# Kernel tuning notes

Hardware: AMD Instinct MI355X
Metric: run time of the kernel (lower is better)

## Reference

```python
import jax, jax.numpy as jnp
import numpy as np

N_META, M_SUB = 64, 1024          # n meta-nodes, m nodes per sub-graph
D_IN, D_HID, D_OUT = 128, 128, 64
NUM_LAYERS_EXTRA, K = 2, 3        # total DSGraphGLayers = NUM_LAYERS_EXTRA + 1
N_EDGES = 1048576                 # ~avg degree 16 over 65536 nodes


def setup_inputs() -> dict:
    key = jax.random.key(0)
    ks = jax.random.split(key, 8)
    N = N_META * M_SUB
    x = jax.random.normal(ks[0], (N_META, M_SUB, D_IN), jnp.float32)
    sub_adj = jax.random.randint(ks[1], (2, N_EDGES), 0, N, dtype=jnp.int32)
    # dense binary meta-graph adjacency (n, n)
    adj = (jax.random.uniform(ks[2], (N_META, N_META)) < 0.1).astype(jnp.float32)
    L = NUM_LAYERS_EXTRA + 1
    scale = 1.0 / np.sqrt(D_HID).astype(np.float32)
    gcn_W = jax.random.normal(ks[3], (L, K + 1, D_HID, D_HID), jnp.float32) * scale
    gcn_b = jnp.zeros((L, K + 1, D_HID), jnp.float32)
    lin_W1 = jax.random.normal(ks[4], (D_HID, D_HID), jnp.float32) * scale
    lin_b1 = jnp.zeros((D_HID,), jnp.float32)
    lin_W2 = jax.random.normal(ks[5], (D_HID, D_OUT), jnp.float32) * scale
    lin_b2 = jnp.zeros((D_OUT,), jnp.float32)
    return dict(x=x, sub_adj=sub_adj, adj=adj, gcn_W=gcn_W, gcn_b=gcn_b,
                lin_W1=lin_W1, lin_b1=lin_b1, lin_W2=lin_W2, lin_b2=lin_b2)


def _gcn_conv(x, src, dst, dinv, W, b, N):
    norm = dinv[src] * dinv[dst]                      # [E+N]
    msg = (x @ W)[src] * norm[:, None]                # [E+N, d_out]
    return jax.ops.segment_sum(msg, dst, num_segments=N) + b


def reference(x, sub_adj, adj, gcn_W, gcn_b, lin_W1, lin_b1, lin_W2, lin_b2):
    n, m, d = x.shape
    N = n * m
    loops = jnp.arange(N, dtype=sub_adj.dtype)
    src = jnp.concatenate([sub_adj[0], loops])
    dst = jnp.concatenate([sub_adj[1], loops])
    deg = jax.ops.segment_sum(jnp.ones(src.shape, x.dtype), dst, num_segments=N)
    dinv = jnp.where(deg > 0, jax.lax.rsqrt(deg), jnp.zeros_like(deg))
    # precompute_adj: cached_adj = [adj, adj^2, ..., adj^K]; powers >= 2 detached in source
    cached = [adj]
    A = adj
    for _ in range(K - 1):
        A = jax.lax.stop_gradient(A @ adj)
        cached.append(A)
    for li in range(gcn_W.shape[0]):
        xf = x.reshape(N, -1)
        out = _gcn_conv(xf, src, dst, dinv, gcn_W[li, 0], gcn_b[li, 0], N)
        for i, Ai in enumerate(cached):
            # meta-graph mixing: x_i[n,m,d] = sum_j A_i[n,j] * x[j,m,d]
            xi = jnp.einsum('nj,jmd->nmd', Ai, x).reshape(N, -1)
            out = out + _gcn_conv(xi, src, dst, dinv, gcn_W[li, i + 1], gcn_b[li, i + 1], N)
        x = jax.nn.relu(out.reshape(n, m, -1))
    h = x.reshape(N, -1)
    h = jax.nn.relu(h @ lin_W1 + lin_b1)
    h = h @ lin_W2 + lin_b2
    return h.reshape(n, m, -1)
```

## Files before the change

### kernel.cpp

```cpp
#include <hip/hip_runtime.h>

#define NMETA 64
#define MSUB 1024
#define NNODES 65536
#define D 128
#define DOUT 64
#define NEDGES 1048576
#define COLS 131072
#define BCAP 5120

typedef __attribute__((ext_vector_type(8))) short bf8_t;
typedef __attribute__((ext_vector_type(4))) float f4_t;
typedef __attribute__((ext_vector_type(2))) float f2_t;

__device__ inline unsigned short bfr(float x) {
    unsigned u = __builtin_bit_cast(unsigned, x);
    u += 0x7fffu + ((u >> 16) & 1u);
    return (unsigned short)(u >> 16);
}
__device__ inline float b2f(unsigned short h) {
    return __builtin_bit_cast(float, (unsigned)h << 16);
}
__device__ inline f2_t up2(unsigned u) {
    f2_t r;
    r[0] = __builtin_bit_cast(float, u << 16);
    r[1] = __builtin_bit_cast(float, u & 0xffff0000u);
    return r;
}

__global__ __launch_bounds__(256) void k_bhist(const int* __restrict__ dst,
                                               int* __restrict__ whist) {
    __shared__ int c[256];
    int t = threadIdx.x, w = blockIdx.x;
    c[t] = 0;
    __syncthreads();
    const int* dp = dst + w * 4096;
    for (int k = 0; k < 16; ++k) atomicAdd(&c[dp[k * 256 + t] >> 8], 1);
    __syncthreads();
    whist[t * 256 + w] = c[t];
}

__global__ __launch_bounds__(256) void k_bscan(int* __restrict__ whist,
                                               int* __restrict__ bbase) {
    __shared__ int sh[256];
    int t = threadIdx.x;
    int run = 0;
    for (int w = 0; w < 256; ++w) {
        int v = whist[t * 256 + w];
        whist[t * 256 + w] = run;
        run += v;
    }
    sh[t] = run;
    __syncthreads();
    for (int d = 1; d < 256; d <<= 1) {
        int x = (t >= d) ? sh[t - d] : 0;
        __syncthreads();
        sh[t] += x;
        __syncthreads();
    }
    bbase[t] = sh[t] - run;
    if (t == 255) bbase[256] = NEDGES;
}

__global__ __launch_bounds__(256) void k_bscatter(const int* __restrict__ src,
                                                  const int* __restrict__ dst,
                                                  const int* __restrict__ bbase,
                                                  const int* __restrict__ whist,
                                                  unsigned* __restrict__ tmp) {
    __shared__ int cur[256];
    __shared__ int base[256];
    int t = threadIdx.x, w = blockIdx.x;
    cur[t] = 0;
    base[t] = bbase[t] + whist[t * 256 + w];
    __syncthreads();
    const int* dp = dst + w * 4096;
    const int* sp = src + w * 4096;
    for (int k = 0; k < 16; ++k) {
        int d = dp[k * 256 + t], s = sp[k * 256 + t];
        int b = d >> 8;
        int lr = atomicAdd(&cur[b], 1);
        tmp[base[b] + lr] = ((unsigned)(d & 255) << 16) | (unsigned)s;
    }
}

__global__ __launch_bounds__(256) void k_bcsr(const unsigned* __restrict__ tmp,
                                              const int* __restrict__ bbase,
                                              int* __restrict__ offs,
                                              float* __restrict__ dinv,
                                              unsigned short* __restrict__ csr16) {
    __shared__ unsigned pairs[BCAP];
    __shared__ unsigned short image[BCAP];
    __shared__ int cnt[256], cur[256], sh[256];
    int t = threadIdx.x, b = blockIdx.x;
    int base = bbase[b], n = bbase[b + 1] - base;
    for (int i = t; i < n; i += 256) pairs[i] = tmp[base + i];
    cnt[t] = 0;
    __syncthreads();
    for (int i = t; i < n; i += 256) atomicAdd(&cnt[pairs[i] >> 16], 1);
    __syncthreads();
    int c = cnt[t];
    sh[t] = c;
    __syncthreads();
    for (int d = 1; d < 256; d <<= 1) {
        int x = (t >= d) ? sh[t - d] : 0;
        __syncthreads();
        sh[t] += x;
        __syncthreads();
    }
    int excl = sh[t] - c;
    cur[t] = excl;
    offs[b * 256 + t] = base + excl;
    dinv[b * 256 + t] = rsqrtf((float)(c + 1));
    if (b == 255 && t == 255) offs[65536] = NEDGES;
    __syncthreads();
    for (int i = t; i < n; i += 256) {
        unsigned p = pairs[i];
        int pos = atomicAdd(&cur[p >> 16], 1);
        image[pos] = (unsigned short)(p & 0xffffu);
    }
    __syncthreads();
    for (int i = t; i < n; i += 256) csr16[base + i] = image[i];
}

__global__ __launch_bounds__(256) void k_setup(const float* __restrict__ A,
                                               unsigned short* __restrict__ Ab,
                                               const float* __restrict__ gcnW,
                                               const float* __restrict__ W1,
                                               const float* __restrict__ W2,
                                               unsigned short* __restrict__ Wt) {
    int blk = blockIdx.x, t = threadIdx.x;
    if (blk == 0) {
        __shared__ float As[4096];
        __shared__ float Bs[4096];
        for (int q = 0; q < 16; ++q) As[t + 256 * q] = A[t + 256 * q];
        __syncthreads();
        for (int q = 0; q < 16; ++q) {
            int idx = t + 256 * q;
            int n = idx >> 6, j = idx & 63;
            Ab[idx] = bfr(As[idx]);
            float acc = 0.f;
            for (int k = 0; k < 64; ++k) acc += As[n * 64 + k] * As[k * 64 + j];
            Bs[idx] = acc;
            Ab[4096 + idx] = bfr(acc);
        }
        __syncthreads();
        for (int q = 0; q < 16; ++q) {
            int idx = t + 256 * q;
            int n = idx >> 6, j = idx & 63;
            float acc = 0.f;
            for (int k = 0; k < 64; ++k) acc += Bs[n * 64 + k] * As[k * 64 + j];
            Ab[8192 + idx] = bfr(acc);
        }
    } else {
        int b2 = blk - 1;
        int m = b2 >> 6;
        int idx = (b2 & 63) * 256 + t;
        const float* src;
        int N = 128;
        if (m < 12)       src = gcnW + m * 16384;
        else if (m == 12) src = W1;
        else { src = W2; N = 64; if (idx >= 8192) return; }
        int n = idx >> 7, k = idx & 127;
        Wt[m * 16384 + idx] = bfr(src[k * N + n]);
    }
}

#define TS 130
template <bool INF32>
__global__ __launch_bounds__(256) void k_layer(const unsigned short* __restrict__ X,
                                               const float* __restrict__ Xf,
                                               const unsigned short* __restrict__ Ab,
                                               const unsigned short* __restrict__ Wt4,
                                               const float* __restrict__ dinv,
                                               unsigned short* __restrict__ Y) {
    __shared__ unsigned short LB[3 * 64 * TS];
    __shared__ float dsh[64];
    int t = threadIdx.x;
    int m = blockIdx.x;
    int wave = t >> 6, lane = t & 63;
    int l16 = lane & 15, kg = lane >> 4;
    int c0 = wave * 32;

    if (t < 64) dsh[t] = dinv[(long)t * MSUB + m];

#pragma unroll
    for (int it = 0; it < 4; ++it) {
        int slot = it * 256 + t;
        int row = slot >> 4, ch = slot & 15;
        if (INF32) {
            const float* xp = Xf + ((long)row * MSUB + m) * D + ch * 8;
            float4 va = *(const float4*)xp;
            float4 vb = *(const float4*)(xp + 4);
            uint4 pk;
            pk.x = ((unsigned)bfr(va.y) << 16) | bfr(va.x);
            pk.y = ((unsigned)bfr(va.w) << 16) | bfr(va.z);
            pk.z = ((unsigned)bfr(vb.y) << 16) | bfr(vb.x);
            pk.w = ((unsigned)bfr(vb.w) << 16) | bfr(vb.z);
            *(uint4*)&LB[row * 128 + ch * 8] = pk;
        } else {
            *(uint4*)&LB[row * 128 + ch * 8] =
                *(const uint4*)(X + ((long)row * MSUB + m) * D + ch * 8);
        }
    }
    __syncthreads();

    bf8_t xa[4][4];
#pragma unroll
    for (int mt = 0; mt < 4; ++mt)
#pragma unroll
        for (int kb = 0; kb < 4; ++kb)
            xa[mt][kb] = *(const bf8_t*)&LB[(mt * 16 + l16) * 128 + kb * 32 + kg * 8];
    __syncthreads();

    f4_t zero4 = {0.f, 0.f, 0.f, 0.f};

    f4_t accT0[4][2];
#pragma unroll
    for (int mt = 0; mt < 4; ++mt)
#pragma unroll
        for (int nt = 0; nt < 2; ++nt) accT0[mt][nt] = zero4;
#pragma unroll
    for (int kb = 0; kb < 4; ++kb)
#pragma unroll
        for (int nt = 0; nt < 2; ++nt) {
            bf8_t b = *(const bf8_t*)(Wt4 + (long)(c0 + nt * 16 + l16) * 128 +
                                      kb * 32 + kg * 8);
#pragma unroll
            for (int mt = 0; mt < 4; ++mt)
                accT0[mt][nt] = __builtin_amdgcn_mfma_f32_16x16x32_bf16(
                    xa[mt][kb], b, accT0[mt][nt], 0, 0, 0);
        }

#pragma unroll
    for (int z = 1; z < 4; ++z) {
        f4_t acc[4][2];
#pragma unroll
        for (int mt = 0; mt < 4; ++mt)
#pragma unroll
            for (int nt = 0; nt < 2; ++nt) acc[mt][nt] = zero4;
        const unsigned short* wp = Wt4 + z * 16384;
#pragma unroll
        for (int kb = 0; kb < 4; ++kb)
#pragma unroll
            for (int nt = 0; nt < 2; ++nt) {
                bf8_t b = *(const bf8_t*)(wp + (long)(c0 + nt * 16 + l16) * 128 +
                                          kb * 32 + kg * 8);
#pragma unroll
                for (int mt = 0; mt < 4; ++mt)
                    acc[mt][nt] = __builtin_amdgcn_mfma_f32_16x16x32_bf16(
                        xa[mt][kb], b, acc[mt][nt], 0, 0, 0);
            }
#pragma unroll
        for (int mt = 0; mt < 4; ++mt)
#pragma unroll
            for (int nt = 0; nt < 2; ++nt)
#pragma unroll
                for (int r = 0; r < 4; ++r)
                    LB[((z - 1) * 64 + mt * 16 + kg * 4 + r) * TS +
                       c0 + nt * 16 + l16] = bfr(acc[mt][nt][r]);
    }

    f4_t acc2[4][2];
#pragma unroll
    for (int mt = 0; mt < 4; ++mt)
#pragma unroll
        for (int nt = 0; nt < 2; ++nt) acc2[mt][nt] = zero4;
#pragma unroll
    for (int i = 0; i < 3; ++i)
#pragma unroll
        for (int kb = 0; kb < 2; ++kb) {
            bf8_t af[4];
#pragma unroll
            for (int mt = 0; mt < 4; ++mt)
                af[mt] = *(const bf8_t*)(Ab + i * 4096 + (mt * 16 + l16) * 64 +
                                         kb * 32 + kg * 8);
#pragma unroll
            for (int nt = 0; nt < 2; ++nt) {
                bf8_t b;
#pragma unroll
                for (int jj = 0; jj < 8; ++jj)
                    b[jj] = (short)LB[(i * 64 + kb * 32 + kg * 8 + jj) * TS +
                                      c0 + nt * 16 + l16];
#pragma unroll
                for (int mt = 0; mt < 4; ++mt)
                    acc2[mt][nt] = __builtin_amdgcn_mfma_f32_16x16x32_bf16(
                        af[mt], b, acc2[mt][nt], 0, 0, 0);
            }
        }

#pragma unroll
    for (int mt = 0; mt < 4; ++mt)
#pragma unroll
        for (int nt = 0; nt < 2; ++nt)
#pragma unroll
            for (int r = 0; r < 4; ++r) {
                int row = mt * 16 + kg * 4 + r;
                int col = c0 + nt * 16 + l16;
                float v = (acc2[mt][nt][r] + accT0[mt][nt][r]) * dsh[row];
                Y[((long)row * MSUB + m) * D + col] = bfr(v);
            }
}

__global__ __launch_bounds__(256) void k_prop(const unsigned short* __restrict__ Y,
                                              const int* __restrict__ offs,
                                              const unsigned short* __restrict__ csr,
                                              const float* __restrict__ dinv,
                                              const float* __restrict__ bias4,
                                              unsigned short* __restrict__ Xout) {
    int wid = threadIdx.x >> 6;
    int lane = threadIdx.x & 63;
    int q = lane >> 4;
    int l = lane & 15;
    int v = blockIdx.x * 4 + wid;
    const uint4* Y4 = (const uint4*)Y;
    int e0 = offs[v], e1 = offs[v + 1];
    f2_t acc2[4];
#pragma unroll
    for (int k = 0; k < 4; ++k) acc2[k] = (f2_t){0.f, 0.f};

    int e = e0 + q;
    for (; e + 12 < e1; e += 16) {
        int u0 = csr[e], u1 = csr[e + 4], u2 = csr[e + 8], u3 = csr[e + 12];
        uint4 y0 = Y4[(long)u0 * 16 + l];
        uint4 y1 = Y4[(long)u1 * 16 + l];
        uint4 y2 = Y4[(long)u2 * 16 + l];
        uint4 y3 = Y4[(long)u3 * 16 + l];
        acc2[0] += (up2(y0.x) + up2(y1.x)) + (up2(y2.x) + up2(y3.x));
        acc2[1] += (up2(y0.y) + up2(y1.y)) + (up2(y2.y) + up2(y3.y));
        acc2[2] += (up2(y0.z) + up2(y1.z)) + (up2(y2.z) + up2(y3.z));
        acc2[3] += (up2(y0.w) + up2(y1.w)) + (up2(y2.w) + up2(y3.w));
    }
    if (e + 4 < e1) {
        int u0 = csr[e], u1 = csr[e + 4];
        uint4 y0 = Y4[(long)u0 * 16 + l];
        uint4 y1 = Y4[(long)u1 * 16 + l];
        acc2[0] += up2(y0.x) + up2(y1.x);
        acc2[1] += up2(y0.y) + up2(y1.y);
        acc2[2] += up2(y0.z) + up2(y1.z);
        acc2[3] += up2(y0.w) + up2(y1.w);
        e += 8;
    }
    if (e < e1) {
        int u = csr[e];
        uint4 y = Y4[(long)u * 16 + l];
        acc2[0] += up2(y.x);
        acc2[1] += up2(y.y);
        acc2[2] += up2(y.z);
        acc2[3] += up2(y.w);
    }
    float acc[8];
#pragma unroll
    for (int k = 0; k < 4; ++k) { acc[2 * k] = acc2[k][0]; acc[2 * k + 1] = acc2[k][1]; }
#pragma unroll
    for (int k = 0; k < 8; ++k) {
        acc[k] += __shfl_xor(acc[k], 32, 64);
        acc[k] += __shfl_xor(acc[k], 16, 64);
    }
    if (q == 0) {
        float dv = dinv[v];
        uint4 s = Y4[(long)v * 16 + l];
        f2_t s2[4] = {up2(s.x), up2(s.y), up2(s.z), up2(s.w)};
        float bs[8];
#pragma unroll
        for (int k = 0; k < 8; ++k) bs[k] = 0.f;
#pragma unroll
        for (int p = 0; p < 4; ++p) {
            float4 blo = *(const float4*)(bias4 + p * 128 + l * 8);
            float4 bhi = *(const float4*)(bias4 + p * 128 + l * 8 + 4);
            bs[0] += blo.x; bs[1] += blo.y; bs[2] += blo.z; bs[3] += blo.w;
            bs[4] += bhi.x; bs[5] += bhi.y; bs[6] += bhi.z; bs[7] += bhi.w;
        }
        unsigned r[8];
#pragma unroll
        for (int k = 0; k < 8; ++k) {
            float sf = s2[k / 2][k % 2];
            r[k] = bfr(fmaxf(dv * (acc[k] + sf) + bs[k], 0.f));
        }
        uint4 pk;
        pk.x = (r[1] << 16) | r[0];
        pk.y = (r[3] << 16) | r[2];
        pk.z = (r[5] << 16) | r[4];
        pk.w = (r[7] << 16) | r[6];
        ((uint4*)Xout)[(long)v * 16 + l] = pk;
    }
}

#define HST 136
__global__ __launch_bounds__(256) void k_mlp(const unsigned short* __restrict__ X,
                                             const unsigned short* __restrict__ Wt,
                                             const float* __restrict__ b1,
                                             const float* __restrict__ b2,
                                             float* __restrict__ out) {
    __shared__ unsigned short H[128 * HST];
    int wave = threadIdx.x >> 6, lane = threadIdx.x & 63;
    int l16 = lane & 15, kg = lane >> 4;
    long row0 = (long)blockIdx.x * 128 + wave * 32;
    int hb = wave * 32 * HST;

    bf8_t a[2][4];
    const unsigned short* xp = X + row0 * 128 + kg * 8;
#pragma unroll
    for (int kb = 0; kb < 4; ++kb) {
        a[0][kb] = *(const bf8_t*)(xp + (long)l16 * 128 + kb * 32);
        a[1][kb] = *(const bf8_t*)(xp + (long)(l16 + 16) * 128 + kb * 32);
    }
    f4_t zero4 = {0.f, 0.f, 0.f, 0.f};
    f4_t acc[2][8];
#pragma unroll
    for (int mt = 0; mt < 2; ++mt)
#pragma unroll
        for (int nt = 0; nt < 8; ++nt) acc[mt][nt] = zero4;

    const unsigned short* wp = Wt + 12 * 16384 + (long)l16 * 128 + kg * 8;
#pragma unroll
    for (int kb = 0; kb < 4; ++kb)
#pragma unroll
        for (int nt = 0; nt < 8; ++nt) {
            bf8_t b = *(const bf8_t*)(wp + nt * 16 * 128 + kb * 32);
            acc[0][nt] = __builtin_amdgcn_mfma_f32_16x16x32_bf16(a[0][kb], b, acc[0][nt], 0, 0, 0);
            acc[1][nt] = __builtin_amdgcn_mfma_f32_16x16x32_bf16(a[1][kb], b, acc[1][nt], 0, 0, 0);
        }

#pragma unroll
    for (int nt = 0; nt < 8; ++nt) {
        float bv = b1[nt * 16 + l16];
#pragma unroll
        for (int mt = 0; mt < 2; ++mt)
#pragma unroll
            for (int r = 0; r < 4; ++r) {
                int row = mt * 16 + kg * 4 + r;
                H[hb + row * HST + nt * 16 + l16] = bfr(fmaxf(acc[mt][nt][r] + bv, 0.f));
            }
    }

    bf8_t h2[2][4];
#pragma unroll
    for (int kb = 0; kb < 4; ++kb) {
        h2[0][kb] = *(const bf8_t*)&H[hb + l16 * HST + kb * 32 + kg * 8];
        h2[1][kb] = *(const bf8_t*)&H[hb + (l16 + 16) * HST + kb * 32 + kg * 8];
    }
    f4_t acc2[2][4];
#pragma unroll
    for (int mt = 0; mt < 2; ++mt)
#pragma unroll
        for (int nt = 0; nt < 4; ++nt) acc2[mt][nt] = zero4;
    const unsigned short* w2 = Wt + 13 * 16384 + (long)l16 * 128 + kg * 8;
#pragma unroll
    for (int kb = 0; kb < 4; ++kb)
#pragma unroll
        for (int nt = 0; nt < 4; ++nt) {
            bf8_t b = *(const bf8_t*)(w2 + nt * 16 * 128 + kb * 32);
            acc2[0][nt] = __builtin_amdgcn_mfma_f32_16x16x32_bf16(h2[0][kb], b, acc2[0][nt], 0, 0, 0);
            acc2[1][nt] = __builtin_amdgcn_mfma_f32_16x16x32_bf16(h2[1][kb], b, acc2[1][nt], 0, 0, 0);
        }
#pragma unroll
    for (int mt = 0; mt < 2; ++mt)
#pragma unroll
        for (int nt = 0; nt < 4; ++nt)
#pragma unroll
            for (int r = 0; r < 4; ++r) {
                long row = row0 + mt * 16 + kg * 4 + r;
                int col = nt * 16 + l16;
                out[row * DOUT + col] = acc2[mt][nt][r] + b2[col];
            }
}

extern "C" void kernel_launch(void* const* d_in, const int* in_sizes, int n_in,
                              void* d_out, int out_size, void* d_ws, size_t ws_size,
                              hipStream_t stream) {
    const float* x      = (const float*)d_in[0];
    const int*   subadj = (const int*)d_in[1];
    const float* adj    = (const float*)d_in[2];
    const float* gcn_W  = (const float*)d_in[3];
    const float* gcn_b  = (const float*)d_in[4];
    const float* lin_W1 = (const float*)d_in[5];
    const float* lin_b1 = (const float*)d_in[6];
    const float* lin_W2 = (const float*)d_in[7];
    const float* lin_b2 = (const float*)d_in[8];
    float* out = (float*)d_out;

    const int* e_src = subadj;
    const int* e_dst = subadj + NEDGES;

    char* w = (char*)d_ws;
    int*      whist = (int*)w;      w += (size_t)65536 * 4;
    int*      bbase = (int*)w;      w += (size_t)260 * 4;
    int*      offs  = (int*)w;      w += (size_t)65540 * 4;
    float*    dinv  = (float*)w;    w += (size_t)65536 * 4;
    unsigned* tmp   = (unsigned*)w; w += (size_t)NEDGES * 4;
    unsigned short* csr16 = (unsigned short*)w; w += (size_t)NEDGES * 2;
    unsigned short* Ab  = (unsigned short*)w; w += (size_t)3 * 4096 * 2;
    unsigned short* Xbf = (unsigned short*)w; w += (size_t)NNODES * D * 2;
    unsigned short* Ybf = (unsigned short*)w; w += (size_t)NNODES * D * 2;
    unsigned short* Wt  = (unsigned short*)w; w += (size_t)14 * 16384 * 2;

    k_bhist<<<256, 256, 0, stream>>>(e_dst, whist);
    k_bscan<<<1, 256, 0, stream>>>(whist, bbase);
    k_bscatter<<<256, 256, 0, stream>>>(e_src, e_dst, bbase, whist, tmp);
    k_bcsr<<<256, 256, 0, stream>>>(tmp, bbase, offs, dinv, csr16);
    k_setup<<<897, 256, 0, stream>>>(adj, Ab, gcn_W, lin_W1, lin_W2, Wt);

    for (int li = 0; li < 3; ++li) {
        if (li == 0)
            k_layer<true><<<MSUB, 256, 0, stream>>>(nullptr, x, Ab, Wt, dinv, Ybf);
        else
            k_layer<false><<<MSUB, 256, 0, stream>>>(Xbf, nullptr, Ab,
                                                     Wt + (size_t)li * 4 * 16384, dinv, Ybf);
        k_prop<<<NNODES / 4, 256, 0, stream>>>(Ybf, offs, csr16, dinv,
                                               gcn_b + (size_t)li * 512, Xbf);
    }
    k_mlp<<<NNODES / 128, 256, 0, stream>>>(Xbf, Wt, lin_b1, lin_b2, out);
}
```

Baseline: 454.8 us.

## Split Y into four 32-column chunks for cache-friendlier sparse propagation

The layer kernel now writes Y as four separate column-chunked arrays, one per wave's 32-column slice, so each chunk covers 65536 nodes by 32 columns. The propagation kernel is re-gridded so each block processes one chunk for 16 nodes and gathers 64-byte rows instead of 256-byte rows. The aim is a smaller working set per gather pass that fits better in L2/MALL. It also adds nontemporal loads and stores for the CSR indices and outputs, at the cost of reading the CSR four times.

```diff
diff --git a/kernel.cpp b/kernel.cpp
--- a/kernel.cpp
+++ b/kernel.cpp
@@ -8,10 +8,12 @@
 #define NEDGES 1048576
 #define COLS 131072
 #define BCAP 5120
+#define YCH (NNODES * 32)
 
 typedef __attribute__((ext_vector_type(8))) short bf8_t;
 typedef __attribute__((ext_vector_type(4))) float f4_t;
 typedef __attribute__((ext_vector_type(2))) float f2_t;
+typedef __attribute__((ext_vector_type(4))) unsigned ui4_t;
 
 __device__ inline unsigned short bfr(float x) {
     unsigned u = __builtin_bit_cast(unsigned, x);
@@ -288,6 +290,7 @@
             }
         }
 
+    unsigned short* Yc = Y + (size_t)wave * YCH;
 #pragma unroll
     for (int mt = 0; mt < 4; ++mt)
 #pragma unroll
@@ -295,9 +298,10 @@
 #pragma unroll
             for (int r = 0; r < 4; ++r) {
                 int row = mt * 16 + kg * 4 + r;
-                int col = c0 + nt * 16 + l16;
+                int cic = nt * 16 + l16;
                 float v = (acc2[mt][nt][r] + accT0[mt][nt][r]) * dsh[row];
-                Y[((long)row * MSUB + m) * D + col] = bfr(v);
+                __builtin_nontemporal_store(
+                    bfr(v), Yc + ((long)row * MSUB + m) * 32 + cic);
             }
 }
 
@@ -307,33 +311,38 @@
                                               const float* __restrict__ dinv,
                                               const float* __restrict__ bias4,
                                               unsigned short* __restrict__ Xout) {
-    int wid = threadIdx.x >> 6;
-    int lane = threadIdx.x & 63;
-    int q = lane >> 4;
-    int l = lane & 15;
-    int v = blockIdx.x * 4 + wid;
-    const uint4* Y4 = (const uint4*)Y;
+    int t = threadIdx.x;
+    int c = blockIdx.x & 3;
+    int v = (blockIdx.x >> 2) * 16 + (t >> 4);
+    int slot = (t >> 2) & 3;
+    int l = t & 3;
+    const uint4* Yc = (const uint4*)(Y + (size_t)c * YCH);
+
     int e0 = offs[v], e1 = offs[v + 1];
     f2_t acc2[4];
 #pragma unroll
     for (int k = 0; k < 4; ++k) acc2[k] = (f2_t){0.f, 0.f};
 
-    int e = e0 + q;
+    int e = e0 + slot;
     for (; e + 12 < e1; e += 16) {
-        int u0 = csr[e], u1 = csr[e + 4], u2 = csr[e + 8], u3 = csr[e + 12];
-        uint4 y0 = Y4[(long)u0 * 16 + l];
-        uint4 y1 = Y4[(long)u1 * 16 + l];
-        uint4 y2 = Y4[(long)u2 * 16 + l];
-        uint4 y3 = Y4[(long)u3 * 16 + l];
+        int u0 = __builtin_nontemporal_load(csr + e);
+        int u1 = __builtin_nontemporal_load(csr + e + 4);
+        int u2 = __builtin_nontemporal_load(csr + e + 8);
+        int u3 = __builtin_nontemporal_load(csr + e + 12);
+        uint4 y0 = Yc[(long)u0 * 4 + l];
+        uint4 y1 = Yc[(long)u1 * 4 + l];
+        uint4 y2 = Yc[(long)u2 * 4 + l];
+        uint4 y3 = Yc[(long)u3 * 4 + l];
         acc2[0] += (up2(y0.x) + up2(y1.x)) + (up2(y2.x) + up2(y3.x));
         acc2[1] += (up2(y0.y) + up2(y1.y)) + (up2(y2.y) + up2(y3.y));
         acc2[2] += (up2(y0.z) + up2(y1.z)) + (up2(y2.z) + up2(y3.z));
         acc2[3] += (up2(y0.w) + up2(y1.w)) + (up2(y2.w) + up2(y3.w));
     }
     if (e + 4 < e1) {
-        int u0 = csr[e], u1 = csr[e + 4];
-        uint4 y0 = Y4[(long)u0 * 16 + l];
-        uint4 y1 = Y4[(long)u1 * 16 + l];
+        int u0 = __builtin_nontemporal_load(csr + e);
+        int u1 = __builtin_nontemporal_load(csr + e + 4);
+        uint4 y0 = Yc[(long)u0 * 4 + l];
+        uint4 y1 = Yc[(long)u1 * 4 + l];
         acc2[0] += up2(y0.x) + up2(y1.x);
         acc2[1] += up2(y0.y) + up2(y1.y);
         acc2[2] += up2(y0.z) + up2(y1.z);
@@ -341,8 +350,8 @@
         e += 8;
     }
     if (e < e1) {
-        int u = csr[e];
-        uint4 y = Y4[(long)u * 16 + l];
+        int u = __builtin_nontemporal_load(csr + e);
+        uint4 y = Yc[(long)u * 4 + l];
         acc2[0] += up2(y.x);
         acc2[1] += up2(y.y);
         acc2[2] += up2(y.z);
@@ -353,20 +362,20 @@
     for (int k = 0; k < 4; ++k) { acc[2 * k] = acc2[k][0]; acc[2 * k + 1] = acc2[k][1]; }
 #pragma unroll
     for (int k = 0; k < 8; ++k) {
-        acc[k] += __shfl_xor(acc[k], 32, 64);
-        acc[k] += __shfl_xor(acc[k], 16, 64);
-    }
-    if (q == 0) {
+        acc[k] += __shfl_xor(acc[k], 4, 64);
+        acc[k] += __shfl_xor(acc[k], 8, 64);
+    }
+    if (slot == 0) {
         float dv = dinv[v];
-        uint4 s = Y4[(long)v * 16 + l];
+        uint4 s = Yc[(long)v * 4 + l];
         f2_t s2[4] = {up2(s.x), up2(s.y), up2(s.z), up2(s.w)};
         float bs[8];
 #pragma unroll
         for (int k = 0; k < 8; ++k) bs[k] = 0.f;
 #pragma unroll
         for (int p = 0; p < 4; ++p) {
-            float4 blo = *(const float4*)(bias4 + p * 128 + l * 8);
-            float4 bhi = *(const float4*)(bias4 + p * 128 + l * 8 + 4);
+            float4 blo = *(const float4*)(bias4 + p * 128 + c * 32 + l * 8);
+            float4 bhi = *(const float4*)(bias4 + p * 128 + c * 32 + l * 8 + 4);
             bs[0] += blo.x; bs[1] += blo.y; bs[2] += blo.z; bs[3] += blo.w;
             bs[4] += bhi.x; bs[5] += bhi.y; bs[6] += bhi.z; bs[7] += bhi.w;
         }
@@ -376,12 +385,13 @@
             float sf = s2[k / 2][k % 2];
             r[k] = bfr(fmaxf(dv * (acc[k] + sf) + bs[k], 0.f));
         }
-        uint4 pk;
+        ui4_t pk;
         pk.x = (r[1] << 16) | r[0];
         pk.y = (r[3] << 16) | r[2];
         pk.z = (r[5] << 16) | r[4];
         pk.w = (r[7] << 16) | r[6];
-        ((uint4*)Xout)[(long)v * 16 + l] = pk;
+        __builtin_nontemporal_store(
+            pk, (ui4_t*)(Xout + (long)v * 128 + c * 32 + l * 8));
     }
 }
 
@@ -506,8 +516,8 @@
         else
             k_layer<false><<<MSUB, 256, 0, stream>>>(Xbf, nullptr, Ab,
                                                      Wt + (size_t)li * 4 * 16384, dinv, Ybf);
-        k_prop<<<NNODES / 4, 256, 0, stream>>>(Ybf, offs, csr16, dinv,
-                                               gcn_b + (size_t)li * 512, Xbf);
+        k_prop<<<(NNODES / 16) * 4, 256, 0, stream>>>(Ybf, offs, csr16, dinv,
+                                                      gcn_b + (size_t)li * 512, Xbf);
     }
     k_mlp<<<NNODES / 128, 256, 0, stream>>>(Xbf, Wt, lin_b1, lin_b2, out);
 }
```

New measurement: 530.1 us. +16.5%, slower.
